# Optimization experiments

Hardware: AMD Instinct MI355X
Metric: run time of the kernel (lower is better)

The kernel has to match this reference:

```python
import jax, jax.numpy as jnp
import numpy as np

B, S, D, H = 4, 2048, 1024, 16
DK = D // H


def setup_inputs() -> dict:
    key = jax.random.key(0)
    ks = jax.random.split(key, 12)
    s = 1.0 / np.sqrt(D)
    return {
        "query": jax.random.normal(ks[0], (B, S, D), jnp.float32),
        "key": jax.random.normal(ks[1], (B, S, D), jnp.float32),
        "value": jax.random.normal(ks[2], (B, S, D), jnp.float32),
        "attention_mask": jax.random.randint(ks[3], (B, S, S), 0, 2, jnp.int32),
        "w_q": jax.random.uniform(ks[4], (D, D), jnp.float32, -s, s),
        "b_q": jax.random.uniform(ks[5], (D,), jnp.float32, -s, s),
        "w_k": jax.random.uniform(ks[6], (D, D), jnp.float32, -s, s),
        "b_k": jax.random.uniform(ks[7], (D,), jnp.float32, -s, s),
        "w_v": jax.random.uniform(ks[8], (D, D), jnp.float32, -s, s),
        "b_v": jax.random.uniform(ks[9], (D,), jnp.float32, -s, s),
        "w_o": jax.random.uniform(ks[10], (D, D), jnp.float32, -s, s),
        "b_o": jax.random.uniform(ks[11], (D,), jnp.float32, -s, s),
    }


def reference(query, key, value, attention_mask, w_q, b_q, w_k, b_k, w_v, b_v, w_o, b_o):
    # project and split heads: [B,S,D] -> [B,H,S,DK]
    def proj(x, w, b):
        y = jnp.einsum('bsd,ed->bse', x, w) + b  # torch Linear: x @ W.T + b
        return y.reshape(B, S, H, DK).transpose(0, 2, 1, 3)

    q = proj(query, w_q, b_q)
    k = proj(key, w_k, b_k)
    v = proj(value, w_v, b_v)

    scores = jnp.einsum('bhqd,bhkd->bhqk', q, k) / np.sqrt(DK).astype(np.float32)
    mask = attention_mask[:, None, :, :]  # broadcast over heads
    scores = jnp.where(mask == 0, jnp.float32(-1e9), scores)
    attn = jax.nn.softmax(scores, axis=-1)  # dropout is identity in eval
    out = jnp.einsum('bhqk,bhkd->bhqd', attn, v)
    out = out.transpose(0, 2, 1, 3).reshape(B, S, D)
    return jnp.einsum('bsd,ed->bse', out, w_o) + b_o
```

## Files before the change

### kernel.cpp

```cpp
#include <hip/hip_runtime.h>


#define B_ 4
#define S_ 2048
#define D_ 1024
#define H_ 16
#define DK_ 64
#define M_ (B_ * S_)

typedef __attribute__((ext_vector_type(4))) float f32x4;
typedef __attribute__((ext_vector_type(8))) short s16x8;
typedef __attribute__((ext_vector_type(8))) unsigned short u16x8;
typedef __attribute__((ext_vector_type(4))) unsigned short u16x4;

__device__ __forceinline__ unsigned short f2bf(float f) {
    union { float f; unsigned int u; } v; v.f = f;
    unsigned int u = v.u;
    return (unsigned short)((u + 0x7FFFu + ((u >> 16) & 1u)) >> 16);
}

__device__ __forceinline__ void gl2lds16(const unsigned short* g, unsigned short* l) {
    __builtin_amdgcn_global_load_lds((const __attribute__((address_space(1))) void*)g,
                                     (__attribute__((address_space(3))) void*)l, 16, 0, 0);
}

__global__ __launch_bounds__(256) void cvt_all(
    const float* __restrict__ q, const float* __restrict__ k, const float* __restrict__ v,
    const float* __restrict__ wq, const float* __restrict__ wk, const float* __restrict__ wv,
    const float* __restrict__ wo,
    unsigned short* __restrict__ Xq, unsigned short* __restrict__ Xk, unsigned short* __restrict__ Xv,
    unsigned short* __restrict__ Wq, unsigned short* __restrict__ Wk, unsigned short* __restrict__ Wv,
    unsigned short* __restrict__ Wo) {
    const int bid = blockIdx.x;
    const float* src;
    unsigned short* dst;
    int blk;
    if (bid < 12288) {
        const int t = bid >> 12;
        blk = bid & 4095;
        src = (t == 0) ? q : ((t == 1) ? k : v);
        dst = (t == 0) ? Xq : ((t == 1) ? Xk : Xv);
    } else {
        const int t = (bid - 12288) >> 9;
        blk = (bid - 12288) & 511;
        src = (t == 0) ? wq : ((t == 1) ? wk : ((t == 2) ? wv : wo));
        dst = (t == 0) ? Wq : ((t == 1) ? Wk : ((t == 2) ? Wv : Wo));
    }
    const int i = (blk * 256 + threadIdx.x) * 8;
    float4 a = *(const float4*)(src + i);
    float4 b = *(const float4*)(src + i + 4);
    u16x8 r;
    r[0] = f2bf(a.x); r[1] = f2bf(a.y); r[2] = f2bf(a.z); r[3] = f2bf(a.w);
    r[4] = f2bf(b.x); r[5] = f2bf(b.y); r[6] = f2bf(b.z); r[7] = f2bf(b.w);
    *(u16x8*)(dst + i) = r;
}

__global__ __launch_bounds__(256) void pack_mask(const int* __restrict__ m,
                                                 unsigned long long* __restrict__ pm) {
    int t = blockIdx.x * 256 + threadIdx.x;
    unsigned long long bits = __ballot(m[t] != 0);
    if ((threadIdx.x & 63) == 0) pm[t >> 6] = bits;
}

template <int MODE>
__global__ __launch_bounds__(256) void gemm_bt(const unsigned short* __restrict__ A,
                                               const unsigned short* __restrict__ Bt,
                                               const float* __restrict__ bias,
                                               float scale, void* __restrict__ Y) {
    __shared__ __align__(16) unsigned short As[128 * 64];
    __shared__ __align__(16) unsigned short Bs[128 * 64];
    const int tid = threadIdx.x;
    const int wave = tid >> 6, lane = tid & 63, quad = lane >> 4, l16 = lane & 15;
    const int m0 = blockIdx.x * 128, n0 = blockIdx.y * 128;
    const int rw = (wave & 1) * 64, cw = (wave >> 1) * 64;
    const int sw = l16 & 7;

    const int srow = tid >> 3, scol = ((tid & 7) ^ (srow & 7)) * 8;
    const unsigned short* ga = A + (size_t)(m0 + srow) * 1024 + scol;
    const unsigned short* gb = Bt + (size_t)(n0 + srow) * 1024 + scol;

    f32x4 acc[4][4];
#pragma unroll
    for (int mi = 0; mi < 4; mi++)
#pragma unroll
        for (int ni = 0; ni < 4; ni++) acc[mi][ni] = (f32x4){0.f, 0.f, 0.f, 0.f};

    for (int k0 = 0; k0 < 1024; k0 += 64) {
#pragma unroll
        for (int r = 0; r < 4; r++) {
            gl2lds16(ga + (size_t)(r * 32) * 1024 + k0, &As[(r * 256 + tid) * 8]);
            gl2lds16(gb + (size_t)(r * 32) * 1024 + k0, &Bs[(r * 256 + tid) * 8]);
        }
        __syncthreads();
#pragma unroll
        for (int kki = 0; kki < 2; kki++) {
            const int xo = ((kki * 4 + quad) ^ sw) * 8;
            s16x8 af[4], bf[4];
#pragma unroll
            for (int mi = 0; mi < 4; mi++)
                af[mi] = *(const s16x8*)&As[(rw + mi * 16 + l16) * 64 + xo];
#pragma unroll
            for (int ni = 0; ni < 4; ni++)
                bf[ni] = *(const s16x8*)&Bs[(cw + ni * 16 + l16) * 64 + xo];
#pragma unroll
            for (int mi = 0; mi < 4; mi++)
#pragma unroll
                for (int ni = 0; ni < 4; ni++)
                    acc[mi][ni] = __builtin_amdgcn_mfma_f32_16x16x32_bf16(af[mi], bf[ni], acc[mi][ni], 0, 0, 0);
        }
        __syncthreads();
    }

    float bv[4];
#pragma unroll
    for (int ni = 0; ni < 4; ni++) bv[ni] = bias[n0 + cw + ni * 16 + l16];
#pragma unroll
    for (int mi = 0; mi < 4; mi++) {
        const int rb = m0 + rw + mi * 16 + quad * 4;
        const int b = rb >> 11, s0 = rb & 2047;
#pragma unroll
        for (int ni = 0; ni < 4; ni++) {
            const int col = n0 + cw + ni * 16 + l16;
            if (MODE == 3) {
#pragma unroll
                for (int i = 0; i < 4; i++)
                    ((float*)Y)[(size_t)(rb + i) * 1024 + col] = (acc[mi][ni][i] + bv[ni]) * scale;
            } else {
                const int h = col >> 6, dk = col & 63;
                if (MODE == 1) {
#pragma unroll
                    for (int i = 0; i < 4; i++)
                        ((unsigned short*)Y)[((size_t)(b * H_ + h) * S_ + s0 + i) * DK_ + dk] =
                            f2bf((acc[mi][ni][i] + bv[ni]) * scale);
                } else {
                    u16x4 pk;
#pragma unroll
                    for (int i = 0; i < 4; i++) pk[i] = f2bf((acc[mi][ni][i] + bv[ni]) * scale);
                    *(u16x4*)&((unsigned short*)Y)[((size_t)(b * H_ + h) * DK_ + dk) * S_ + s0] = pk;
                }
            }
        }
    }
}

__global__ __launch_bounds__(256) void attn_kernel(const unsigned short* __restrict__ Q,
                                                   const unsigned short* __restrict__ K,
                                                   const unsigned short* __restrict__ Vt,
                                                   const unsigned long long* __restrict__ pm,
                                                   unsigned short* __restrict__ ctx) {
    __shared__ __align__(16) unsigned short Ks[2][64 * 64];
    __shared__ __align__(16) unsigned short Vs[2][64 * 64];
    __shared__ __align__(16) unsigned short Ps[8 * 16 * 64];

    const int tid = threadIdx.x;
    const int wave = tid >> 6, lane = tid & 63, quad = lane >> 4, l16 = lane & 15;
    const int bh = blockIdx.y, b = bh >> 4, h = bh & 15;
    const int q0 = blockIdx.x * 128;
    const int qbase = q0 + wave * 32;
    const int sw = l16 & 7, q4 = quad * 4, qh = quad >> 1;

    const unsigned short* Kbase = K + (size_t)bh * S_ * DK_;
    const unsigned short* Vbase = Vt + (size_t)bh * DK_ * S_;

    s16x8 qf[2][2];
#pragma unroll
    for (int qb = 0; qb < 2; qb++) {
        const unsigned short* qr = Q + ((size_t)bh * S_ + qbase + qb * 16 + l16) * DK_ + quad * 8;
        qf[qb][0] = *(const s16x8*)qr;
        qf[qb][1] = *(const s16x8*)(qr + 32);
    }
    const unsigned long long* pmq[2];
#pragma unroll
    for (int qb = 0; qb < 2; qb++)
        pmq[qb] = pm + ((size_t)b * S_ + qbase + qb * 16 + l16) * 32;

    s16x8 ones;
#pragma unroll
    for (int j = 0; j < 8; j++) ones[j] = (short)0x3F80;

    f32x4 oacc[2][4], lacc[2];
#pragma unroll
    for (int qb = 0; qb < 2; qb++) {
        lacc[qb] = (f32x4){0.f, 0.f, 0.f, 0.f};
#pragma unroll
        for (int ct = 0; ct < 4; ct++) oacc[qb][ct] = (f32x4){0.f, 0.f, 0.f, 0.f};
    }

    const int sr = tid >> 3, sc = ((tid & 7) ^ (sr & 7)) * 8;
    const unsigned short* Kg0 = Kbase + (size_t)sr * DK_ + sc;
    const unsigned short* Kg1 = Kbase + (size_t)(32 + sr) * DK_ + sc;
    const unsigned short* Vg0 = Vbase + (size_t)sr * S_ + sc;
    const unsigned short* Vg1 = Vbase + (size_t)(32 + sr) * S_ + sc;

    gl2lds16(Kg0, &Ks[0][tid * 8]);
    gl2lds16(Kg1, &Ks[0][2048 + tid * 8]);
    gl2lds16(Vg0, &Vs[0][tid * 8]);
    gl2lds16(Vg1, &Vs[0][2048 + tid * 8]);

    for (int kt = 0; kt < S_ / 64; kt++) {
        const int cur = kt & 1;

        uint2 mv[2];
        mv[0] = *(const uint2*)&pmq[0][kt];
        mv[1] = *(const uint2*)&pmq[1][kt];
        __builtin_amdgcn_sched_barrier(0);

        if (kt + 1 < S_ / 64) {
            const int k1 = (kt + 1) * 64;
            const int nb = cur ^ 1;
            gl2lds16(Kg0 + (size_t)k1 * DK_, &Ks[nb][tid * 8]);
            gl2lds16(Kg1 + (size_t)k1 * DK_, &Ks[nb][2048 + tid * 8]);
            gl2lds16(Vg0 + k1, &Vs[nb][tid * 8]);
            gl2lds16(Vg1 + k1, &Vs[nb][2048 + tid * 8]);
            asm volatile("s_waitcnt vmcnt(4)" ::: "memory");
        } else {
            asm volatile("s_waitcnt vmcnt(0)" ::: "memory");
        }
        __builtin_amdgcn_s_barrier();

        f32x4 sacc[2][4];
#pragma unroll
        for (int qb = 0; qb < 2; qb++)
#pragma unroll
            for (int ct = 0; ct < 4; ct++) sacc[qb][ct] = (f32x4){0.f, 0.f, 0.f, 0.f};
#pragma unroll
        for (int kki = 0; kki < 2; kki++) {
            const int xo = ((kki * 4 + quad) ^ sw) * 8;
            s16x8 kf[4];
#pragma unroll
            for (int ct = 0; ct < 4; ct++)
                kf[ct] = *(const s16x8*)&Ks[cur][(ct * 16 + l16) * 64 + xo];
            __builtin_amdgcn_s_setprio(1);
#pragma unroll
            for (int qb = 0; qb < 2; qb++)
#pragma unroll
                for (int ct = 0; ct < 4; ct++)
                    sacc[qb][ct] = __builtin_amdgcn_mfma_f32_16x16x32_bf16(kf[ct], qf[qb][kki], sacc[qb][ct], 0, 0, 0);
            __builtin_amdgcn_s_setprio(0);
        }

#pragma unroll
        for (int qb = 0; qb < 2; qb++) {
            unsigned short* pwq = &Ps[(wave * 2 + qb) * 1024];
            const unsigned mqx = mv[qb].x >> q4;
            const unsigned mqy = mv[qb].y >> q4;
#pragma unroll
            for (int ct = 0; ct < 4; ct++) {
                const unsigned mq = (ct & 2) ? mqy : mqx;
                unsigned pu[4];
#pragma unroll
                for (int i = 0; i < 4; i++) {
                    const int pos = (ct & 1) * 16 + i;
                    const int mb = __builtin_amdgcn_sbfe(mq, pos, 1);
                    const float p = exp2f(sacc[qb][ct][i]);
                    pu[i] = __float_as_uint(p) & (unsigned)mb;
                }
                const int ch = ((2 * ct + qh) ^ sw) * 8;
#pragma unroll
                for (int t = 0; t < 2; t++) {
                    const unsigned pk = __builtin_amdgcn_perm(pu[2 * t + 1], pu[2 * t], 0x07060302u);
                    *(unsigned*)&pwq[l16 * 64 + ch + ((q4 + 2 * t) & 7)] = pk;
                }
            }
        }

#pragma unroll
        for (int kki = 0; kki < 2; kki++) {
            const int xo = ((kki * 4 + quad) ^ sw) * 8;
            s16x8 vf[4];
#pragma unroll
            for (int ct = 0; ct < 4; ct++)
                vf[ct] = *(const s16x8*)&Vs[cur][(ct * 16 + l16) * 64 + xo];
#pragma unroll
            for (int qb = 0; qb < 2; qb++) {
                s16x8 pf = *(const s16x8*)&Ps[(wave * 2 + qb) * 1024 + l16 * 64 + xo];
                __builtin_amdgcn_s_setprio(1);
#pragma unroll
                for (int ct = 0; ct < 4; ct++)
                    oacc[qb][ct] = __builtin_amdgcn_mfma_f32_16x16x32_bf16(pf, vf[ct], oacc[qb][ct], 0, 0, 0);
                lacc[qb] = __builtin_amdgcn_mfma_f32_16x16x32_bf16(pf, ones, lacc[qb], 0, 0, 0);
                __builtin_amdgcn_s_setprio(0);
            }
        }

        asm volatile("s_waitcnt lgkmcnt(0)" ::: "memory");
        __builtin_amdgcn_s_barrier();
    }

#pragma unroll
    for (int qb = 0; qb < 2; qb++) {
        f32x4 rl;
#pragma unroll
        for (int i = 0; i < 4; i++) rl[i] = 1.0f / lacc[qb][i];
#pragma unroll
        for (int ct = 0; ct < 4; ct++) {
            const int col = h * DK_ + ct * 16 + l16;
#pragma unroll
            for (int i = 0; i < 4; i++) {
                const int sg = qbase + qb * 16 + quad * 4 + i;
                ctx[((size_t)(b * S_ + sg)) * D_ + col] = f2bf(oacc[qb][ct][i] * rl[i]);
            }
        }
    }
}

extern "C" void kernel_launch(void* const* d_in, const int* in_sizes, int n_in,
                              void* d_out, int out_size, void* d_ws, size_t ws_size,
                              hipStream_t stream) {
    const float* query = (const float*)d_in[0];
    const float* key   = (const float*)d_in[1];
    const float* value = (const float*)d_in[2];
    const int*   mask  = (const int*)d_in[3];
    const float* w_q = (const float*)d_in[4];
    const float* b_q = (const float*)d_in[5];
    const float* w_k = (const float*)d_in[6];
    const float* b_k = (const float*)d_in[7];
    const float* w_v = (const float*)d_in[8];
    const float* b_v = (const float*)d_in[9];
    const float* w_o = (const float*)d_in[10];
    const float* b_o = (const float*)d_in[11];

    char* ws = (char*)d_ws;
    const size_t XSZ = (size_t)M_ * D_ * 2;
    const size_t WSZ = (size_t)D_ * D_ * 2;
    unsigned short* Xq  = (unsigned short*)(ws);
    unsigned short* Xk  = (unsigned short*)(ws + XSZ);
    unsigned short* Xv  = (unsigned short*)(ws + 2 * XSZ);
    unsigned short* Wq  = (unsigned short*)(ws + 3 * XSZ);
    unsigned short* Wk  = (unsigned short*)(ws + 3 * XSZ + WSZ);
    unsigned short* Wv  = (unsigned short*)(ws + 3 * XSZ + 2 * WSZ);
    unsigned short* Wo  = (unsigned short*)(ws + 3 * XSZ + 3 * WSZ);
    unsigned short* Qb  = (unsigned short*)(ws + 3 * XSZ + 4 * WSZ);
    unsigned short* Kb  = (unsigned short*)(ws + 4 * XSZ + 4 * WSZ);
    unsigned short* Vtb = (unsigned short*)(ws + 5 * XSZ + 4 * WSZ);
    unsigned short* ctx = (unsigned short*)(ws + 6 * XSZ + 4 * WSZ);
    unsigned long long* pm = (unsigned long long*)(ws);

    hipLaunchKernelGGL(cvt_all, dim3(14336), dim3(256), 0, stream,
                       query, key, value, w_q, w_k, w_v, w_o,
                       Xq, Xk, Xv, Wq, Wk, Wv, Wo);

    const float QSCALE = 0.125f * 1.44269504f;
    dim3 ggrid(M_ / 128, D_ / 128);
    hipLaunchKernelGGL(HIP_KERNEL_NAME(gemm_bt<1>), ggrid, dim3(256), 0, stream, Xq, Wq, b_q, QSCALE, (void*)Qb);
    hipLaunchKernelGGL(HIP_KERNEL_NAME(gemm_bt<1>), ggrid, dim3(256), 0, stream, Xk, Wk, b_k, 1.0f, (void*)Kb);
    hipLaunchKernelGGL(HIP_KERNEL_NAME(gemm_bt<2>), ggrid, dim3(256), 0, stream, Xv, Wv, b_v, 1.0f, (void*)Vtb);

    hipLaunchKernelGGL(pack_mask, dim3((B_ * S_ * S_) / 256), dim3(256), 0, stream, mask, pm);

    hipLaunchKernelGGL(attn_kernel, dim3(S_ / 128, B_ * H_), dim3(256), 0, stream,
                       Qb, Kb, Vtb, pm, ctx);

    hipLaunchKernelGGL(HIP_KERNEL_NAME(gemm_bt<3>), ggrid, dim3(256), 0, stream, ctx, Wo, b_o, 1.0f, d_out);
}
```

Measured before the change: 456.0 us.

## Keep softmax probabilities in registers via permlane swaps instead of LDS round-trip

The P tile (exp of scores, masked and packed to bf16) is no longer written to shared memory and read back as the A operand of the PV MFMA. The MFMA output layout is instead converted to input layout with v_permlane32_swap and v_permlane16_swap cross-lane swaps. The change also uses the raw hardware exp2 builtin in place of exp2f. This removes LDS stores and loads and the shared-memory footprint for P, which may help occupancy, at the cost of more live registers and a correctness dependency on the lane mapping of the swaps.

```diff
diff --git a/kernel.cpp b/kernel.cpp
--- a/kernel.cpp
+++ b/kernel.cpp
@@ -150,14 +150,13 @@
                                                    unsigned short* __restrict__ ctx) {
     __shared__ __align__(16) unsigned short Ks[2][64 * 64];
     __shared__ __align__(16) unsigned short Vs[2][64 * 64];
-    __shared__ __align__(16) unsigned short Ps[8 * 16 * 64];
 
     const int tid = threadIdx.x;
     const int wave = tid >> 6, lane = tid & 63, quad = lane >> 4, l16 = lane & 15;
     const int bh = blockIdx.y, b = bh >> 4, h = bh & 15;
     const int q0 = blockIdx.x * 128;
     const int qbase = q0 + wave * 32;
-    const int sw = l16 & 7, q4 = quad * 4, qh = quad >> 1;
+    const int sw = l16 & 7, q4 = quad * 4;
 
     const unsigned short* Kbase = K + (size_t)bh * S_ * DK_;
     const unsigned short* Vbase = Vt + (size_t)bh * DK_ * S_;
@@ -239,27 +238,24 @@
             __builtin_amdgcn_s_setprio(0);
         }
 
+        unsigned pk[2][4][2];
 #pragma unroll
         for (int qb = 0; qb < 2; qb++) {
-            unsigned short* pwq = &Ps[(wave * 2 + qb) * 1024];
             const unsigned mqx = mv[qb].x >> q4;
             const unsigned mqy = mv[qb].y >> q4;
 #pragma unroll
             for (int ct = 0; ct < 4; ct++) {
                 const unsigned mq = (ct & 2) ? mqy : mqx;
-                unsigned pu[4];
-#pragma unroll
-                for (int i = 0; i < 4; i++) {
-                    const int pos = (ct & 1) * 16 + i;
-                    const int mb = __builtin_amdgcn_sbfe(mq, pos, 1);
-                    const float p = exp2f(sacc[qb][ct][i]);
-                    pu[i] = __float_as_uint(p) & (unsigned)mb;
-                }
-                const int ch = ((2 * ct + qh) ^ sw) * 8;
 #pragma unroll
                 for (int t = 0; t < 2; t++) {
-                    const unsigned pk = __builtin_amdgcn_perm(pu[2 * t + 1], pu[2 * t], 0x07060302u);
-                    *(unsigned*)&pwq[l16 * 64 + ch + ((q4 + 2 * t) & 7)] = pk;
+                    const int pos = (ct & 1) * 16 + 2 * t;
+                    const int mb0 = __builtin_amdgcn_sbfe(mq, pos, 1);
+                    const int mb1 = __builtin_amdgcn_sbfe(mq, pos + 1, 1);
+                    const unsigned p0 =
+                        __float_as_uint(__builtin_amdgcn_exp2f(sacc[qb][ct][2 * t])) & (unsigned)mb0;
+                    const unsigned p1 =
+                        __float_as_uint(__builtin_amdgcn_exp2f(sacc[qb][ct][2 * t + 1])) & (unsigned)mb1;
+                    pk[qb][ct][t] = __builtin_amdgcn_perm(p1, p0, 0x07060302u);
                 }
             }
         }
@@ -273,7 +269,15 @@
                 vf[ct] = *(const s16x8*)&Vs[cur][(ct * 16 + l16) * 64 + xo];
 #pragma unroll
             for (int qb = 0; qb < 2; qb++) {
-                s16x8 pf = *(const s16x8*)&Ps[(wave * 2 + qb) * 1024 + l16 * 64 + xo];
+                unsigned w0 = pk[qb][2 * kki][0], w2 = pk[qb][2 * kki + 1][0];
+                unsigned w1 = pk[qb][2 * kki][1], w3 = pk[qb][2 * kki + 1][1];
+                asm("v_permlane32_swap_b32 %0, %1" : "+v"(w0), "+v"(w2));
+                asm("v_permlane16_swap_b32 %0, %1" : "+v"(w0), "+v"(w2));
+                asm("v_permlane32_swap_b32 %0, %1" : "+v"(w1), "+v"(w3));
+                asm("v_permlane16_swap_b32 %0, %1" : "+v"(w1), "+v"(w3));
+                union { unsigned u[4]; s16x8 v; } pfu;
+                pfu.u[0] = w0; pfu.u[1] = w1; pfu.u[2] = w2; pfu.u[3] = w3;
+                const s16x8 pf = pfu.v;
                 __builtin_amdgcn_s_setprio(1);
 #pragma unroll
                 for (int ct = 0; ct < 4; ct++)
```

Result: faster. 430.6 us (-5.6%).
